# Optimization experiments

Hardware: AMD Instinct MI355X
Metric: run time of the kernel (lower is better)

The kernel has to match this reference:

```python
import jax, jax.numpy as jnp
import numpy as np

B, S, D = 2, 2048, 2048
H, KVH, HD = 16, 4, 128
R = 128
WINDOW, GLOBAL = 512, 64
THETA = 1000000.0


def setup_inputs() -> dict:
    key = jax.random.key(0)
    ks = jax.random.split(key, 13)
    def rn(k, shape, s=0.02):
        return jax.random.normal(k, shape, dtype=jnp.float32) * s
    return {
        'x': jax.random.normal(ks[0], (B, S, D), dtype=jnp.float32),
        'wq_w': rn(ks[1], (H * HD, D)), 'wq_a': rn(ks[2], (R, D)), 'wq_b': rn(ks[3], (H * HD, R)),
        'wk_w': rn(ks[4], (KVH * HD, D)), 'wk_a': rn(ks[5], (R, D)), 'wk_b': rn(ks[6], (KVH * HD, R)),
        'wv_w': rn(ks[7], (KVH * HD, D)), 'wv_a': rn(ks[8], (R, D)), 'wv_b': rn(ks[9], (KVH * HD, R)),
        'wo_w': rn(ks[10], (D, H * HD)), 'wo_a': rn(ks[11], (R, H * HD)), 'wo_b': rn(ks[12], (D, R)),
    }


def _lora_linear(x, w, a, b):
    # F.linear(x, w) + F.linear(F.linear(x, A), B)
    return x @ w.T + (x @ a.T) @ b.T


def _apply_rope(x, cos, sin):
    # view_as_complex pairs consecutive elements: (x0,x1),(x2,x3),...
    xr, xi = x[..., 0::2], x[..., 1::2]
    out_r = xr * cos - xi * sin
    out_i = xr * sin + xi * cos
    return jnp.stack([out_r, out_i], axis=-1).reshape(x.shape)


def reference(x, wq_w, wq_a, wq_b, wk_w, wk_a, wk_b, wv_w, wv_a, wv_b, wo_w, wo_a, wo_b):
    # RoPE frequencies (scaling_factor=1.0 -> plain RoPE; YaRN ramp is identity)
    inv_freq = 1.0 / (THETA ** (jnp.arange(0, HD, 2, dtype=jnp.float32) / HD))
    t = jnp.arange(S, dtype=jnp.float32)
    freqs = t[:, None] * inv_freq[None, :]           # [S, HD/2]
    cos = jnp.cos(freqs)[None, :, None, :]           # [1,S,1,HD/2]
    sin = jnp.sin(freqs)[None, :, None, :]

    q = _lora_linear(x, wq_w, wq_a, wq_b).reshape(B, S, H, HD)
    k = _lora_linear(x, wk_w, wk_a, wk_b).reshape(B, S, KVH, HD)
    v = _lora_linear(x, wv_w, wv_a, wv_b).reshape(B, S, KVH, HD)

    q = _apply_rope(q, cos, sin)
    k = _apply_rope(k, cos, sin)

    # GQA: repeat kv heads
    g = H // KVH
    k = jnp.repeat(k, g, axis=2)
    v = jnp.repeat(v, g, axis=2)

    scores = jnp.einsum('bqhd,bkhd->bhqk', q, k) / jnp.sqrt(jnp.float32(HD))
    i = jnp.arange(S)[:, None]
    j = jnp.arange(S)[None, :]
    # causal + local sliding window + global tokens (attended by all)
    allowed = (j <= i) & (((i - j) < WINDOW) | (j < GLOBAL))
    scores = jnp.where(allowed[None, None], scores, jnp.float32(-1e9))
    p = jax.nn.softmax(scores, axis=-1)
    out = jnp.einsum('bhqk,bkhd->bqhd', p, v).reshape(B, S, H * HD)
    return _lora_linear(out, wo_w, wo_a, wo_b)
```

## Files before the change

kernel.cpp:

```cpp
#include <hip/hip_runtime.h>

#define B_ 2
#define S_LEN 2048
#define DMODEL 2048
#define NH 16
#define NKVH 4
#define HD 128
#define RLORA 128
#define WINDOW_ 512
#define NGLOBAL 64

#define FENCE asm volatile("" ::: "memory")

typedef __bf16 bf16x8 __attribute__((ext_vector_type(8)));
typedef float f32x4 __attribute__((ext_vector_type(4)));

__device__ __forceinline__ float bf2f(unsigned short h) {
    return __uint_as_float(((unsigned int)h) << 16);
}
__device__ __forceinline__ unsigned short f2bf(float f) {
    unsigned int u = __float_as_uint(f);
    unsigned int r = u + 0x7fffu + ((u >> 16) & 1u);
    return (unsigned short)(r >> 16);
}
__device__ __forceinline__ unsigned int pack2bf(float a, float b) {
    return (unsigned int)f2bf(a) | ((unsigned int)f2bf(b) << 16);
}
__device__ __forceinline__ uint4 load8f(const float* p) {
    float4 f0 = *(const float4*)p;
    float4 f1 = *(const float4*)(p + 4);
    uint4 u;
    u.x = pack2bf(f0.x, f0.y);
    u.y = pack2bf(f0.z, f0.w);
    u.z = pack2bf(f1.x, f1.y);
    u.w = pack2bf(f1.z, f1.w);
    return u;
}

__device__ __forceinline__ void gld16(const unsigned short* g, unsigned short* l) {
    __builtin_amdgcn_global_load_lds(
        (const __attribute__((address_space(1))) unsigned int*)g,
        (__attribute__((address_space(3))) unsigned int*)l,
        16, 0, 0);
}

struct Conv12 {
    const float* s[12];
    unsigned short* d[12];
    int c[13];
};
__global__ __launch_bounds__(256) void convk(Conv12 a)
{
    int b = blockIdx.x;
    int seg = 0;
    while (b >= a.c[seg + 1]) seg++;
    int off = (b - a.c[seg]) * 2048 + threadIdx.x * 8;
    *(uint4*)(a.d[seg] + off) = load8f(a.s[seg] + off);
}

struct TransA4 { const float* s[4]; unsigned short* d[4]; };
__global__ __launch_bounds__(256) void transAk(TransA4 a)
{
    __shared__ float tile[32][65];
    const int bid = blockIdx.x;
    const int mat = bid >> 7;
    const int tl = bid & 127;
    const int rt = tl & 3, ct = tl >> 2;
    const float* src = a.s[mat];
    unsigned short* dst = a.d[mat];
    const int t = threadIdx.x;
    #pragma unroll
    for (int p = 0; p < 2; p++) {
        int r = p * 16 + (t >> 4);
        int c = (t & 15) * 4;
        float4 v = *(const float4*)(src + (size_t)(rt * 32 + r) * 2048 + ct * 64 + c);
        tile[r][c] = v.x; tile[r][c + 1] = v.y;
        tile[r][c + 2] = v.z; tile[r][c + 3] = v.w;
    }
    __syncthreads();
    const int n = t >> 2, r8 = (t & 3) * 8;
    uint4 u;
    u.x = pack2bf(tile[r8 + 0][n], tile[r8 + 1][n]);
    u.y = pack2bf(tile[r8 + 2][n], tile[r8 + 3][n]);
    u.z = pack2bf(tile[r8 + 4][n], tile[r8 + 5][n]);
    u.w = pack2bf(tile[r8 + 6][n], tile[r8 + 7][n]);
    *(uint4*)(dst + (size_t)(ct * 64 + n) * 128 + rt * 32 + r8) = u;
}

__global__ __launch_bounds__(256) void weffk(
    unsigned short* __restrict__ C, int ldc,
    const unsigned short* __restrict__ Bm,
    const unsigned short* __restrict__ At,
    int seg)
{
    const int m0 = blockIdx.x * 128;
    const int n0 = blockIdx.y * 128;
    const unsigned short* Atb = At;
    if (seg)
        Atb = At + ((m0 < 2048) ? 0 : (m0 < 2560) ? (2048 * 128) : (2 * 2048 * 128));
    __shared__ __align__(16) unsigned short As_[128 * 32];
    __shared__ __align__(16) unsigned short Bs_[128 * 32];
    const int tid = threadIdx.x, lane = tid & 63, wid = tid >> 6;
    const int quad = lane >> 4, l16 = lane & 15;
    const int lr = lane >> 2, lc8 = (lane & 3) * 8;
    const int wm0 = (wid >> 1) * 64, wn0 = (wid & 1) * 64;
    f32x4 acc[4][4] = {};
    for (int k0 = 0; k0 < 128; k0 += 32) {
        #pragma unroll
        for (int c = 0; c < 2; c++) {
            int chunk = wid * 2 + c;
            gld16(Bm + (size_t)(m0 + chunk * 16 + lr) * 128 + k0 + lc8, As_ + chunk * 512);
            gld16(Atb + (size_t)(n0 + chunk * 16 + lr) * 128 + k0 + lc8, Bs_ + chunk * 512);
        }
        __syncthreads();
        bf16x8 af[4], bf[4];
        #pragma unroll
        for (int i = 0; i < 4; i++)
            af[i] = *(const bf16x8*)&As_[(wm0 + i * 16 + l16) * 32 + quad * 8];
        #pragma unroll
        for (int j = 0; j < 4; j++)
            bf[j] = *(const bf16x8*)&Bs_[(wn0 + j * 16 + l16) * 32 + quad * 8];
        #pragma unroll
        for (int i = 0; i < 4; i++)
            #pragma unroll
            for (int j = 0; j < 4; j++)
                acc[i][j] = __builtin_amdgcn_mfma_f32_16x16x32_bf16(af[i], bf[j], acc[i][j], 0, 0, 0);
        __syncthreads();
    }
    #pragma unroll
    for (int i = 0; i < 4; i++)
        #pragma unroll
        for (int j = 0; j < 4; j++) {
            const int col = n0 + wn0 + j * 16 + l16;
            #pragma unroll
            for (int r = 0; r < 4; r++) {
                size_t idx = (size_t)(m0 + wm0 + i * 16 + quad * 4 + r) * ldc + col;
                C[idx] = f2bf(bf2f(C[idx]) + acc[i][j][r]);
            }
        }
}

__device__ __forceinline__ void gemm128_acc(
    const unsigned short* __restrict__ A, int lda, int m0,
    const unsigned short* __restrict__ W, int ldw, int n0,
    int Kmain, f32x4 (&acc)[4][4])
{
    __shared__ __align__(16) unsigned short As[2][128 * 32];
    __shared__ __align__(16) unsigned short Bs[2][256 * 32];
    const int tid = threadIdx.x;
    const int lane = tid & 63, wid = tid >> 6;
    const int quad = lane >> 4, l16 = lane & 15;
    const int wm = (wid >> 2) * 64, wn = (wid & 3) * 64;

    const int arow = tid >> 2;
    const int acol = (((tid & 3) * 16) ^ (((arow >> 1) & 3) << 4)) >> 1;

    const int nt = Kmain >> 5;

    auto stage = [&](int bb, int j) {
        const int k0 = j << 5;
        gld16(A + (size_t)(m0 + arow) * lda + k0 + acol, &As[bb][tid * 8]);
        gld16(W + (size_t)(n0 + arow) * ldw + k0 + acol, &Bs[bb][tid * 8]);
        gld16(W + (size_t)(n0 + arow + 128) * ldw + k0 + acol, &Bs[bb][tid * 8 + 4096]);
    };

    const int xoff = (((quad * 16) ^ (((l16 >> 1) & 3) << 4)) >> 1);
    const int ard = (wm + l16) * 32 + xoff;
    const int brd = (wn + l16) * 32 + xoff;

    stage(0, 0);
    stage(1, 1);

    for (int t = 0; t < nt; t++) {
        const int bb = t & 1;
        if (t < nt - 1) {
            asm volatile("s_waitcnt vmcnt(3)" ::: "memory");
        } else {
            asm volatile("s_waitcnt vmcnt(0)" ::: "memory");
        }
        __builtin_amdgcn_sched_barrier(0);
        FENCE; __builtin_amdgcn_s_barrier(); FENCE;

        bf16x8 af[4], bfn[4];
        #pragma unroll
        for (int mi = 0; mi < 4; mi++)
            af[mi] = *(const bf16x8*)&As[bb][ard + mi * 512];
        #pragma unroll
        for (int ni = 0; ni < 4; ni++)
            bfn[ni] = *(const bf16x8*)&Bs[bb][brd + ni * 512];

        __builtin_amdgcn_s_setprio(1);
        #pragma unroll
        for (int mi = 0; mi < 4; mi++)
            #pragma unroll
            for (int ni = 0; ni < 4; ni++)
                acc[mi][ni] = __builtin_amdgcn_mfma_f32_16x16x32_bf16(
                    af[mi], bfn[ni], acc[mi][ni], 0, 0, 0);
        __builtin_amdgcn_s_setprio(0);

        FENCE; __builtin_amdgcn_s_barrier(); FENCE;
        if (t + 2 < nt) stage(bb, t + 2);
    }
}

__global__ __launch_bounds__(512, 4) void gemm128_qkv(
    const unsigned short* __restrict__ Xb,
    const unsigned short* __restrict__ Wqkv,
    unsigned short* __restrict__ Qo, unsigned short* __restrict__ Ko,
    unsigned short* __restrict__ Vt)
{
    const int m0 = blockIdx.x * 128;
    const int n0 = blockIdx.y * 256;
    f32x4 acc[4][4] = {};
    gemm128_acc(Xb, DMODEL, m0, Wqkv, DMODEL, n0, DMODEL, acc);

    const int tid = threadIdx.x, lane = tid & 63, wid = tid >> 6;
    const int l16 = lane & 15, quad = lane >> 4;
    const int wm = (wid >> 2) * 64, wn = (wid & 3) * 64;

    if (n0 < 2048) {
        #pragma unroll
        for (int mi = 0; mi < 4; mi++)
            #pragma unroll
            for (int ni = 0; ni < 4; ni++) {
                const int col = n0 + wn + ni * 16 + l16;
                const size_t rb = (size_t)(m0 + wm + mi * 16 + quad * 4);
                #pragma unroll
                for (int r = 0; r < 4; r++)
                    Qo[(rb + r) * DMODEL + col] = f2bf(acc[mi][ni][r]);
            }
    } else if (n0 < 2560) {
        #pragma unroll
        for (int mi = 0; mi < 4; mi++)
            #pragma unroll
            for (int ni = 0; ni < 4; ni++) {
                const int col = n0 - 2048 + wn + ni * 16 + l16;
                const size_t rb = (size_t)(m0 + wm + mi * 16 + quad * 4);
                #pragma unroll
                for (int r = 0; r < 4; r++)
                    Ko[(rb + r) * 512 + col] = f2bf(acc[mi][ni][r]);
            }
    } else {
        const int b = m0 >> 11;
        #pragma unroll
        for (int mi = 0; mi < 4; mi++)
            #pragma unroll
            for (int ni = 0; ni < 4; ni++) {
                const int ncol = n0 - 2560 + wn + ni * 16 + l16;
                const int head = ncol >> 7, dd = ncol & 127;
                const int srow = (m0 & (S_LEN - 1)) + wm + mi * 16 + quad * 4;
                uint2 pk;
                pk.x = pack2bf(acc[mi][ni][0], acc[mi][ni][1]);
                pk.y = pack2bf(acc[mi][ni][2], acc[mi][ni][3]);
                *(uint2*)(Vt + ((size_t)(b * NKVH + head) * HD + dd) * S_LEN + srow) = pk;
            }
    }
}

__global__ __launch_bounds__(512, 4) void gemm128_out(
    const unsigned short* __restrict__ Xb,
    const unsigned short* __restrict__ Ww,
    float* __restrict__ Out)
{
    const int m0 = blockIdx.x * 128;
    const int n0 = blockIdx.y * 256;
    f32x4 acc[4][4] = {};
    gemm128_acc(Xb, DMODEL, m0, Ww, DMODEL, n0, DMODEL, acc);

    const int tid = threadIdx.x, lane = tid & 63, wid = tid >> 6;
    const int l16 = lane & 15, quad = lane >> 4;
    const int wm = (wid >> 2) * 64, wn = (wid & 3) * 64;
    #pragma unroll
    for (int mi = 0; mi < 4; mi++)
        #pragma unroll
        for (int ni = 0; ni < 4; ni++) {
            const int col = n0 + wn + ni * 16 + l16;
            const size_t rb = (size_t)(m0 + wm + mi * 16 + quad * 4);
            #pragma unroll
            for (int r = 0; r < 4; r++)
                Out[(rb + r) * DMODEL + col] = acc[mi][ni][r];
        }
}

__global__ __launch_bounds__(256) void rope_vec_k(
    unsigned short* __restrict__ Qb, unsigned short* __restrict__ Kb)
{
    int idx = blockIdx.x * 256 + threadIdx.x;
    const int npq = (B_ * S_LEN) * NH * 16;
    unsigned short* ptr;
    int m, tg;
    if (idx < npq) {
        tg = idx & 15;
        int h = (idx >> 4) & (NH - 1);
        m = idx >> 8;
        ptr = Qb + (size_t)m * (NH * HD) + h * HD + tg * 8;
    } else {
        idx -= npq;
        if (idx >= (B_ * S_LEN) * NKVH * 16) return;
        tg = idx & 15;
        int h = (idx >> 4) & (NKVH - 1);
        m = idx >> 6;
        ptr = Kb + (size_t)m * (NKVH * HD) + h * HD + tg * 8;
    }
    float pos = (float)(m & (S_LEN - 1));
    uint4 u = *(const uint4*)ptr;
    unsigned int w[4] = {u.x, u.y, u.z, u.w};
    #pragma unroll
    for (int j = 0; j < 4; j++) {
        int t = tg * 4 + j;
        float inv_freq = __expf(-(float)t * (13.815510557964274f / 64.0f));
        float ang = pos * inv_freq;
        float c, s;
        __sincosf(ang, &s, &c);
        float xr = __uint_as_float(w[j] << 16);
        float xi = __uint_as_float(w[j] & 0xffff0000u);
        w[j] = pack2bf(xr * c - xi * s, xr * s + xi * c);
    }
    *(uint4*)ptr = make_uint4(w[0], w[1], w[2], w[3]);
}

__global__ __launch_bounds__(256, 2) void attn_mfma(
    const unsigned short* __restrict__ Q,
    const unsigned short* __restrict__ K,
    const unsigned short* __restrict__ Vt,
    unsigned short* __restrict__ O)
{
    __shared__ __align__(16) unsigned short kvbuf[2][8192];
    __shared__ unsigned short plds[4][32 * 40];
    const int tid = threadIdx.x, lane = tid & 63, wid = tid >> 6;
    const int l16 = lane & 15, quad = lane >> 4;
    const int bid = blockIdx.x;
    const int g   = bid & 7;
    const int kvh = g & 3;
    const int b   = g >> 2;
    const int qt  = 63 - (bid >> 3);
    const int q0  = qt * 32;
    const int h   = kvh * 4 + wid;

    const unsigned short* qrow0 = Q + ((size_t)(b * S_LEN + q0 + l16)) * DMODEL + h * HD;
    bf16x8 qf0[4], qf1[4];
    #pragma unroll
    for (int c = 0; c < 4; c++) {
        qf0[c] = *(const bf16x8*)(qrow0 + c * 32 + quad * 8);
        qf1[c] = *(const bf16x8*)(qrow0 + (size_t)16 * DMODEL + c * 32 + quad * 8);
    }

    const unsigned short* Kbase  = K + ((size_t)(b * S_LEN)) * (NKVH * HD) + kvh * HD;
    const unsigned short* Vplane = Vt + ((size_t)(b * NKVH + kvh) * HD) * S_LEN;
    unsigned short* pw = &plds[wid][0];

    const unsigned short* Ksrc[2];
    const unsigned short* Vsrc[2];
    #pragma unroll
    for (int c = 0; c < 2; c++) {
        const int o = wid * 2048 + c * 1024 + lane * 16;
        const int kkey = o >> 8;
        const int kdim = (o & 255) ^ ((kkey & 15) << 4);
        Ksrc[c] = Kbase + (size_t)kkey * (NKVH * HD) + (kdim >> 1);
        const int vd = o >> 6;
        const int vkb = (o & 63) ^ ((vd & 3) << 4);
        Vsrc[c] = Vplane + (size_t)vd * S_LEN + (vkb >> 1);
    }

    f32x4 oacc0[8] = {}, oacc1[8] = {};
    f32x4 lrow0 = {0.f, 0.f, 0.f, 0.f}, lrow1 = {0.f, 0.f, 0.f, 0.f};
    const float c2 = 0.12753102f;

    const int kthi = (q0 + 31) >> 5;
    int wlo = q0 - (WINDOW_ - 1); if (wlo < 0) wlo = 0;
    const int ktw = wlo >> 5;

    auto nexttile = [&](int t) -> int {
        if (t < ktw) { int u = t + 1; return (u < 2 && u < ktw) ? u : ktw; }
        return t + 1;
    };

    auto stage = [&](int buf, int ktb) {
        #pragma unroll
        for (int c = 0; c < 2; c++) {
            gld16(Ksrc[c] + (size_t)ktb * (NKVH * HD),
                  &kvbuf[buf][wid * 1024 + c * 512]);
            gld16(Vsrc[c] + ktb,
                  &kvbuf[buf][4096 + wid * 1024 + c * 512]);
        }
    };

    int kt = 0;
    stage(0, 0);
    __syncthreads();
    int cur = 0;

    while (true) {
        const int ktb = kt * 32;
        const int ktn = nexttile(kt);
        const bool last = (ktn > kthi);
        if (!last) stage(cur ^ 1, ktn * 32);

        const unsigned short* kb  = kvbuf[cur];
        const unsigned short* vbp = kvbuf[cur] + 4096;

        bf16x8 kf0[4], kf1[4];
        #pragma unroll
        for (int c = 0; c < 4; c++) {
            const int koff = (l16 * 256 + ((c * 64 + quad * 16) ^ (l16 << 4))) >> 1;
            kf0[c] = *(const bf16x8*)&kb[koff];
            kf1[c] = *(const bf16x8*)&kb[koff + 2048];
        }

        f32x4 s00 = {}, s01 = {}, s10 = {}, s11 = {};
        __builtin_amdgcn_s_setprio(1);
        #pragma unroll
        for (int c = 0; c < 4; c++) {
            s00 = __builtin_amdgcn_mfma_f32_16x16x32_bf16(qf0[c], kf0[c], s00, 0, 0, 0);
            s01 = __builtin_amdgcn_mfma_f32_16x16x32_bf16(qf0[c], kf1[c], s01, 0, 0, 0);
            s10 = __builtin_amdgcn_mfma_f32_16x16x32_bf16(qf1[c], kf0[c], s10, 0, 0, 0);
            s11 = __builtin_amdgcn_mfma_f32_16x16x32_bf16(qf1[c], kf1[c], s11, 0, 0, 0);
        }
        __builtin_amdgcn_s_setprio(0);

        #pragma unroll
        for (int s = 0; s < 2; s++) {
            const f32x4 sa0 = s ? s10 : s00;
            const f32x4 sa1 = s ? s11 : s01;
            const int qs = q0 + s * 16;
            const bool full = (ktb + 31 <= qs) &&
                              (((qs + 15) - ktb < WINDOW_) || (ktb + 31 < NGLOBAL));
            f32x4& lr = s ? lrow1 : lrow0;
            #pragma unroll
            for (int rr = 0; rr < 4; rr++) {
                float p0 = exp2f(sa0[rr] * c2);
                float p1 = exp2f(sa1[rr] * c2);
                if (!full) {
                    const int i = qs + quad * 4 + rr;
                    const int j0 = ktb + l16, j1 = j0 + 16;
                    bool a0 = (j0 <= i) && ((i - j0 < WINDOW_) || (j0 < NGLOBAL));
                    bool a1 = (j1 <= i) && ((i - j1 < WINDOW_) || (j1 < NGLOBAL));
                    p0 = a0 ? p0 : 0.f;
                    p1 = a1 ? p1 : 0.f;
                }
                lr[rr] += p0 + p1;
                pw[(s * 16 + quad * 4 + rr) * 40 + l16]      = f2bf(p0);
                pw[(s * 16 + quad * 4 + rr) * 40 + 16 + l16] = f2bf(p1);
            }
        }
        bf16x8 pa0 = *(const bf16x8*)(pw + l16 * 40 + quad * 8);
        bf16x8 pa1 = *(const bf16x8*)(pw + (16 + l16) * 40 + quad * 8);

        {
            bf16x8 va[4];
            #pragma unroll
            for (int ds = 0; ds < 4; ds++) {
                const int d = ds * 16 + l16;
                va[ds] = *(const bf16x8*)&vbp[(d * 64 + ((quad * 16) ^ ((l16 & 3) << 4))) >> 1];
            }
            __builtin_amdgcn_s_setprio(1);
            #pragma unroll
            for (int ds = 0; ds < 4; ds++) {
                oacc0[ds] = __builtin_amdgcn_mfma_f32_16x16x32_bf16(pa0, va[ds], oacc0[ds], 0, 0, 0);
                oacc1[ds] = __builtin_amdgcn_mfma_f32_16x16x32_bf16(pa1, va[ds], oacc1[ds], 0, 0, 0);
            }
            __builtin_amdgcn_s_setprio(0);
        }
        {
            bf16x8 vb[4];
            #pragma unroll
            for (int ds = 0; ds < 4; ds++) {
                const int d = (ds + 4) * 16 + l16;
                vb[ds] = *(const bf16x8*)&vbp[(d * 64 + ((quad * 16) ^ ((l16 & 3) << 4))) >> 1];
            }
            __builtin_amdgcn_s_setprio(1);
            #pragma unroll
            for (int ds = 0; ds < 4; ds++) {
                oacc0[ds + 4] = __builtin_amdgcn_mfma_f32_16x16x32_bf16(pa0, vb[ds], oacc0[ds + 4], 0, 0, 0);
                oacc1[ds + 4] = __builtin_amdgcn_mfma_f32_16x16x32_bf16(pa1, vb[ds], oacc1[ds + 4], 0, 0, 0);
            }
            __builtin_amdgcn_s_setprio(0);
        }

        if (last) break;
        __syncthreads();
        cur ^= 1;
        kt = ktn;
    }

    #pragma unroll
    for (int off = 1; off <= 8; off <<= 1) {
        #pragma unroll
        for (int rr = 0; rr < 4; rr++) {
            lrow0[rr] += __shfl_xor(lrow0[rr], off);
            lrow1[rr] += __shfl_xor(lrow1[rr], off);
        }
    }

    #pragma unroll
    for (int s = 0; s < 2; s++) {
        const f32x4& lr = s ? lrow1 : lrow0;
        #pragma unroll
        for (int rr = 0; rr < 4; rr++) {
            float inv = 1.f / lr[rr];
            unsigned short* orow = O + ((size_t)(b * S_LEN + q0 + s * 16 + quad * 4 + rr)) * DMODEL + h * HD;
            #pragma unroll
            for (int ds = 0; ds < 8; ds++) {
                float v = s ? oacc1[ds][rr] : oacc0[ds][rr];
                orow[ds * 16 + l16] = f2bf(v * inv);
            }
        }
    }
}

extern "C" void kernel_launch(void* const* d_in, const int* in_sizes, int n_in,
                              void* d_out, int out_size, void* d_ws, size_t ws_size,
                              hipStream_t stream)
{
    const float* x    = (const float*)d_in[0];
    const float* wq_w = (const float*)d_in[1];
    const float* wq_a = (const float*)d_in[2];
    const float* wq_b = (const float*)d_in[3];
    const float* wk_w = (const float*)d_in[4];
    const float* wk_a = (const float*)d_in[5];
    const float* wk_b = (const float*)d_in[6];
    const float* wv_w = (const float*)d_in[7];
    const float* wv_a = (const float*)d_in[8];
    const float* wv_b = (const float*)d_in[9];
    const float* wo_w = (const float*)d_in[10];
    const float* wo_a = (const float*)d_in[11];
    const float* wo_b = (const float*)d_in[12];

    char* ws = (char*)d_ws;
    unsigned short* wqkvb  = (unsigned short*)(ws);
    unsigned short* apackT = (unsigned short*)(ws + 12582912);
    unsigned short* bqkvb  = (unsigned short*)(ws + 14155776);
    unsigned short* Qbuf   = (unsigned short*)(ws + 18087936);
    unsigned short* Kbuf   = (unsigned short*)(ws + 34865152);
    unsigned short* Vtbuf  = (unsigned short*)(ws + 39059456);
    unsigned short* wowb   = (unsigned short*)(ws);
    unsigned short* wobb   = (unsigned short*)(ws + 8388608);
    unsigned short* woabT  = (unsigned short*)(ws + 8912896);
    unsigned short* xb = (unsigned short*)d_out;

    Conv12 c1;
    c1.s[0] = x;    c1.d[0] = xb;
    c1.s[1] = wq_w; c1.d[1] = wqkvb;
    c1.s[2] = wk_w; c1.d[2] = wqkvb + 2048 * 2048;
    c1.s[3] = wv_w; c1.d[3] = wqkvb + 2560 * 2048;
    c1.s[4] = wq_b; c1.d[4] = bqkvb;
    c1.s[5] = wk_b; c1.d[5] = bqkvb + 2048 * 128;
    c1.s[6] = wv_b; c1.d[6] = bqkvb + 2560 * 128;
    for (int i = 7; i < 12; i++) { c1.s[i] = wv_b; c1.d[i] = bqkvb + 2560 * 128; }
    int cum1[13] = {0, 4096, 6144, 6656, 7168, 7296, 7328, 7360, 7360, 7360,
                    7360, 7360, 7360};
    for (int i = 0; i < 13; i++) c1.c[i] = cum1[i];
    convk<<<dim3(7360), dim3(256), 0, stream>>>(c1);

    TransA4 t1;
    t1.s[0] = wq_a; t1.d[0] = apackT;
    t1.s[1] = wk_a; t1.d[1] = apackT + 2048 * 128;
    t1.s[2] = wv_a; t1.d[2] = apackT + 2 * 2048 * 128;
    t1.s[3] = wq_a; t1.d[3] = apackT;
    transAk<<<dim3(384), dim3(256), 0, stream>>>(t1);

    weffk<<<dim3(24, 16), dim3(256), 0, stream>>>(wqkvb, DMODEL, bqkvb, apackT, 1);

    gemm128_qkv<<<dim3(32, 12), dim3(512), 0, stream>>>(
        xb, wqkvb, Qbuf, Kbuf, Vtbuf);

    Conv12 c2;
    c2.s[0] = wo_w; c2.d[0] = wowb;
    c2.s[1] = wo_b; c2.d[1] = wobb;
    for (int i = 2; i < 12; i++) { c2.s[i] = wo_b; c2.d[i] = wobb; }
    int cum2[13] = {0, 2048, 2176, 2176, 2176, 2176, 2176, 2176, 2176, 2176,
                    2176, 2176, 2176};
    for (int i = 0; i < 13; i++) c2.c[i] = cum2[i];
    convk<<<dim3(2176), dim3(256), 0, stream>>>(c2);

    TransA4 t2;
    t2.s[0] = wo_a; t2.d[0] = woabT;
    t2.s[1] = wo_a; t2.d[1] = woabT;
    t2.s[2] = wo_a; t2.d[2] = woabT;
    t2.s[3] = wo_a; t2.d[3] = woabT;
    transAk<<<dim3(128), dim3(256), 0, stream>>>(t2);

    weffk<<<dim3(16, 16), dim3(256), 0, stream>>>(wowb, DMODEL, wobb, woabT, 0);

    rope_vec_k<<<dim3(5120), dim3(256), 0, stream>>>(Qbuf, Kbuf);

    attn_mfma<<<dim3(512), dim3(256), 0, stream>>>(Qbuf, Kbuf, Vtbuf, Qbuf);

    gemm128_out<<<dim3(32, 8), dim3(512), 0, stream>>>(
        Qbuf, wowb, (float*)d_out);
}
```

Measured before the change: 336.4 us.

## Fuse RoPE into QKV GEMM epilogue and shrink GEMM tiles to 128x128

Applies rotary embedding inside the QKV projection epilogue, using lane shuffles to pair real and imaginary columns, and removes the standalone rope kernel and its extra read/write pass over Q and K. The shared GEMM routine also moves from 128x256 tiles with 512 threads to 128x128 tiles with 256 threads, doubling the grid for better CU occupancy. In exchange, each tile reuses less data and the epilogue does extra sincos work.

```diff
diff --git a/kernel.cpp b/kernel.cpp
--- a/kernel.cpp
+++ b/kernel.cpp
@@ -145,23 +145,33 @@
     const unsigned short* __restrict__ W, int ldw, int n0,
     int Kmain, f32x4 (&acc)[4][4])
 {
-    __shared__ __align__(16) unsigned short As[2][128 * 32];
-    __shared__ __align__(16) unsigned short Bs[2][256 * 32];
+    __shared__ __align__(16) unsigned short As[2][4096];
+    __shared__ __align__(16) unsigned short Bs[2][4096];
     const int tid = threadIdx.x;
     const int lane = tid & 63, wid = tid >> 6;
     const int quad = lane >> 4, l16 = lane & 15;
-    const int wm = (wid >> 2) * 64, wn = (wid & 3) * 64;
-
-    const int arow = tid >> 2;
-    const int acol = (((tid & 3) * 16) ^ (((arow >> 1) & 3) << 4)) >> 1;
+    const int wm = (wid >> 1) * 64, wn = (wid & 1) * 64;
+
+    int arow[2], acol[2];
+    #pragma unroll
+    for (int c = 0; c < 2; c++) {
+        const int o = tid * 16 + c * 4096;
+        arow[c] = o >> 6;
+        acol[c] = (((tid & 3) * 16) ^ (((arow[c] >> 1) & 3) << 4)) >> 1;
+    }
 
     const int nt = Kmain >> 5;
 
     auto stage = [&](int bb, int j) {
         const int k0 = j << 5;
-        gld16(A + (size_t)(m0 + arow) * lda + k0 + acol, &As[bb][tid * 8]);
-        gld16(W + (size_t)(n0 + arow) * ldw + k0 + acol, &Bs[bb][tid * 8]);
-        gld16(W + (size_t)(n0 + arow + 128) * ldw + k0 + acol, &Bs[bb][tid * 8 + 4096]);
+        #pragma unroll
+        for (int c = 0; c < 2; c++)
+            gld16(A + (size_t)(m0 + arow[c]) * lda + k0 + acol[c],
+                  &As[bb][tid * 8 + c * 2048]);
+        #pragma unroll
+        for (int c = 0; c < 2; c++)
+            gld16(W + (size_t)(n0 + arow[c]) * ldw + k0 + acol[c],
+                  &Bs[bb][tid * 8 + c * 2048]);
     };
 
     const int xoff = (((quad * 16) ^ (((l16 >> 1) & 3) << 4)) >> 1);
@@ -174,7 +184,7 @@
     for (int t = 0; t < nt; t++) {
         const int bb = t & 1;
         if (t < nt - 1) {
-            asm volatile("s_waitcnt vmcnt(3)" ::: "memory");
+            asm volatile("s_waitcnt vmcnt(4)" ::: "memory");
         } else {
             asm volatile("s_waitcnt vmcnt(0)" ::: "memory");
         }
@@ -203,20 +213,38 @@
     }
 }
 
-__global__ __launch_bounds__(512, 4) void gemm128_qkv(
+__device__ __forceinline__ f32x4 rope4(f32x4 v, int col, int rowbase)
+{
+    const int t2 = col & 127;
+    const float invf = __expf(-(float)(t2 >> 1) * (13.815510557964274f / 64.0f));
+    const bool ev = (t2 & 1) == 0;
+    f32x4 o;
+    #pragma unroll
+    for (int r = 0; r < 4; r++) {
+        float self = v[r];
+        float other = __shfl_xor(self, 1);
+        float pos = (float)((rowbase + r) & (S_LEN - 1));
+        float s, c;
+        __sincosf(pos * invf, &s, &c);
+        o[r] = ev ? (self * c - other * s) : (other * s + self * c);
+    }
+    return o;
+}
+
+__global__ __launch_bounds__(256, 3) void gemm128_qkv(
     const unsigned short* __restrict__ Xb,
     const unsigned short* __restrict__ Wqkv,
     unsigned short* __restrict__ Qo, unsigned short* __restrict__ Ko,
     unsigned short* __restrict__ Vt)
 {
     const int m0 = blockIdx.x * 128;
-    const int n0 = blockIdx.y * 256;
+    const int n0 = blockIdx.y * 128;
     f32x4 acc[4][4] = {};
     gemm128_acc(Xb, DMODEL, m0, Wqkv, DMODEL, n0, DMODEL, acc);
 
     const int tid = threadIdx.x, lane = tid & 63, wid = tid >> 6;
     const int l16 = lane & 15, quad = lane >> 4;
-    const int wm = (wid >> 2) * 64, wn = (wid & 3) * 64;
+    const int wm = (wid >> 1) * 64, wn = (wid & 1) * 64;
 
     if (n0 < 2048) {
         #pragma unroll
@@ -224,10 +252,11 @@
             #pragma unroll
             for (int ni = 0; ni < 4; ni++) {
                 const int col = n0 + wn + ni * 16 + l16;
-                const size_t rb = (size_t)(m0 + wm + mi * 16 + quad * 4);
+                const int rb = m0 + wm + mi * 16 + quad * 4;
+                f32x4 v = rope4(acc[mi][ni], col, rb);
                 #pragma unroll
                 for (int r = 0; r < 4; r++)
-                    Qo[(rb + r) * DMODEL + col] = f2bf(acc[mi][ni][r]);
+                    Qo[(size_t)(rb + r) * DMODEL + col] = f2bf(v[r]);
             }
     } else if (n0 < 2560) {
         #pragma unroll
@@ -235,10 +264,11 @@
             #pragma unroll
             for (int ni = 0; ni < 4; ni++) {
                 const int col = n0 - 2048 + wn + ni * 16 + l16;
-                const size_t rb = (size_t)(m0 + wm + mi * 16 + quad * 4);
+                const int rb = m0 + wm + mi * 16 + quad * 4;
+                f32x4 v = rope4(acc[mi][ni], col, rb);
                 #pragma unroll
                 for (int r = 0; r < 4; r++)
-                    Ko[(rb + r) * 512 + col] = f2bf(acc[mi][ni][r]);
+                    Ko[(size_t)(rb + r) * 512 + col] = f2bf(v[r]);
             }
     } else {
         const int b = m0 >> 11;
@@ -257,19 +287,19 @@
     }
 }
 
-__global__ __launch_bounds__(512, 4) void gemm128_out(
+__global__ __launch_bounds__(256, 3) void gemm128_out(
     const unsigned short* __restrict__ Xb,
     const unsigned short* __restrict__ Ww,
     float* __restrict__ Out)
 {
     const int m0 = blockIdx.x * 128;
-    const int n0 = blockIdx.y * 256;
+    const int n0 = blockIdx.y * 128;
     f32x4 acc[4][4] = {};
     gemm128_acc(Xb, DMODEL, m0, Ww, DMODEL, n0, DMODEL, acc);
 
     const int tid = threadIdx.x, lane = tid & 63, wid = tid >> 6;
     const int l16 = lane & 15, quad = lane >> 4;
-    const int wm = (wid >> 2) * 64, wn = (wid & 3) * 64;
+    const int wm = (wid >> 1) * 64, wn = (wid & 1) * 64;
     #pragma unroll
     for (int mi = 0; mi < 4; mi++)
         #pragma unroll
@@ -280,43 +310,6 @@
             for (int r = 0; r < 4; r++)
                 Out[(rb + r) * DMODEL + col] = acc[mi][ni][r];
         }
-}
-
-__global__ __launch_bounds__(256) void rope_vec_k(
-    unsigned short* __restrict__ Qb, unsigned short* __restrict__ Kb)
-{
-    int idx = blockIdx.x * 256 + threadIdx.x;
-    const int npq = (B_ * S_LEN) * NH * 16;
-    unsigned short* ptr;
-    int m, tg;
-    if (idx < npq) {
-        tg = idx & 15;
-        int h = (idx >> 4) & (NH - 1);
-        m = idx >> 8;
-        ptr = Qb + (size_t)m * (NH * HD) + h * HD + tg * 8;
-    } else {
-        idx -= npq;
-        if (idx >= (B_ * S_LEN) * NKVH * 16) return;
-        tg = idx & 15;
-        int h = (idx >> 4) & (NKVH - 1);
-        m = idx >> 6;
-        ptr = Kb + (size_t)m * (NKVH * HD) + h * HD + tg * 8;
-    }
-    float pos = (float)(m & (S_LEN - 1));
-    uint4 u = *(const uint4*)ptr;
-    unsigned int w[4] = {u.x, u.y, u.z, u.w};
-    #pragma unroll
-    for (int j = 0; j < 4; j++) {
-        int t = tg * 4 + j;
-        float inv_freq = __expf(-(float)t * (13.815510557964274f / 64.0f));
-        float ang = pos * inv_freq;
-        float c, s;
-        __sincosf(ang, &s, &c);
-        float xr = __uint_as_float(w[j] << 16);
-        float xi = __uint_as_float(w[j] & 0xffff0000u);
-        w[j] = pack2bf(xr * c - xi * s, xr * s + xi * c);
-    }
-    *(uint4*)ptr = make_uint4(w[0], w[1], w[2], w[3]);
 }
 
 __global__ __launch_bounds__(256, 2) void attn_mfma(
@@ -561,7 +554,7 @@
 
     weffk<<<dim3(24, 16), dim3(256), 0, stream>>>(wqkvb, DMODEL, bqkvb, apackT, 1);
 
-    gemm128_qkv<<<dim3(32, 12), dim3(512), 0, stream>>>(
+    gemm128_qkv<<<dim3(32, 24), dim3(256), 0, stream>>>(
         xb, wqkvb, Qbuf, Kbuf, Vtbuf);
 
     Conv12 c2;
@@ -582,10 +575,8 @@
 
     weffk<<<dim3(16, 16), dim3(256), 0, stream>>>(wowb, DMODEL, wobb, woabT, 0);
 
-    rope_vec_k<<<dim3(5120), dim3(256), 0, stream>>>(Qbuf, Kbuf);
-
     attn_mfma<<<dim3(512), dim3(256), 0, stream>>>(Qbuf, Kbuf, Vtbuf, Qbuf);
 
-    gemm128_out<<<dim3(32, 8), dim3(512), 0, stream>>>(
+    gemm128_out<<<dim3(32, 16), dim3(256), 0, stream>>>(
         Qbuf, wowb, (float*)d_out);
 }
```

After: 317.0 us. 5.8% less time.
